# Kernel optimization log

Hardware: AMD Instinct MI355X
Metric: run time of the kernel (lower is better)

The kernel has to match this reference:

```python
import jax, jax.numpy as jnp
import numpy as np

T, B, D, H = 512, 64, 512, 512  # seq_len, batch, input_size, hidden_size


def setup_inputs() -> dict:
    key = jax.random.key(0)
    ks = jax.random.split(key, 7)
    s = 1.0 / np.sqrt(H)
    return {
        "input": jax.random.normal(ks[0], (T, B, D), dtype=jnp.float32),
        "h0": jax.random.normal(ks[1], (B, H), dtype=jnp.float32),
        "c0": jax.random.normal(ks[2], (B, H), dtype=jnp.float32),
        "W_ih": jax.random.normal(ks[3], (4 * H, D), dtype=jnp.float32) * s,
        "W_hh": jax.random.normal(ks[4], (4 * H, H), dtype=jnp.float32) * s,
        "b_ih": jax.random.normal(ks[5], (4 * H,), dtype=jnp.float32) * s,
        "b_hh": jax.random.normal(ks[6], (4 * H,), dtype=jnp.float32) * s,
        "batch_first": 0,
    }


def reference(input, h0, c0, W_ih, W_hh, b_ih, b_hh, batch_first):
    # Dense (non-packed) branch of RNNLayer.forward with an LSTM cell.
    x = jnp.swapaxes(input, 0, 1) if batch_first else input  # [T, B, D]
    # Input projection is independent of the recurrence: precompute for all t.
    x_proj = jnp.einsum('tbd,gd->tbg', x, W_ih) + b_ih  # [T, B, 4H]

    def step(carry, xt):
        h, c = carry
        gates = xt + h @ W_hh.T + b_hh  # [B, 4H]
        i, f, g, o = jnp.split(gates, 4, axis=-1)
        c_new = jax.nn.sigmoid(f) * c + jax.nn.sigmoid(i) * jnp.tanh(g)
        h_new = jax.nn.sigmoid(o) * jnp.tanh(c_new)
        return (h_new, c_new), h_new

    (hT, cT), ys = jax.lax.scan(step, (h0, c0), x_proj)  # ys: [T, B, H]
    outputs = jnp.swapaxes(ys, 0, 1) if batch_first else ys
    return outputs, hT, cT
```

## Files before the change

### kernel.cpp

```cpp
#include <hip/hip_runtime.h>

typedef __attribute__((ext_vector_type(8))) short bfrag;
typedef __attribute__((ext_vector_type(4))) float f32x4;
typedef __attribute__((ext_vector_type(4))) int i32x4;

#define NT 512
#define NB 64
#define KD 512
#define NG 2048
#define GB 4
#define GH 16

#define YS_SZ (NT * NB * KD)
#define HT_OFF YS_SZ
#define CT_OFF (YS_SZ + NB * KD)

__device__ __forceinline__ unsigned short f2bf(float f) {
  unsigned u = __float_as_uint(f);
  u += 0x7fffu + ((u >> 16) & 1u);
  return (unsigned short)(u >> 16);
}
__device__ __forceinline__ float bf2f(unsigned short h) {
  return __uint_as_float(((unsigned)h) << 16);
}
__device__ __forceinline__ float sigm(float v) { return 1.f / (1.f + __expf(-v)); }
__device__ __forceinline__ float tanh_f(float v) { return 1.f - 2.f / (__expf(2.f * v) + 1.f); }

__global__ __launch_bounds__(256) void cvt_bf16(const float* __restrict__ src,
                                                unsigned short* __restrict__ dst, int n8) {
  int i = blockIdx.x * 256 + threadIdx.x;
  if (i >= n8) return;
  const float4 a = *(const float4*)(src + (size_t)i * 8);
  const float4 b = *(const float4*)(src + (size_t)i * 8 + 4);
  i32x4 v;
  v.x = (int)(f2bf(a.x) | ((unsigned)f2bf(a.y) << 16));
  v.y = (int)(f2bf(a.z) | ((unsigned)f2bf(a.w) << 16));
  v.z = (int)(f2bf(b.x) | ((unsigned)f2bf(b.y) << 16));
  v.w = (int)(f2bf(b.z) | ((unsigned)f2bf(b.w) << 16));
  *(i32x4*)(dst + (size_t)i * 8) = v;
}

template <int XP32>
__global__ __launch_bounds__(256) void xproj_gemm(const unsigned short* __restrict__ Wb,
                                                  const unsigned short* __restrict__ Xb,
                                                  const float* __restrict__ bias,
                                                  void* __restrict__ XPv) {
  __shared__ unsigned short Wt[64 * 40];
  __shared__ unsigned short Xt[64 * 40];
  const int tid = threadIdx.x;
  const int lane = tid & 63, wid = tid >> 6;
  const int g = lane >> 4, cc = lane & 15;
  const int n0 = blockIdx.x * 64;
  const int t = blockIdx.y;
  const size_t m0 = (size_t)t * 64;
  const int srow = tid >> 2, schunk = (tid & 3) * 8;

  f32x4 acc[4] = {};
  for (int kb = 0; kb < KD; kb += 32) {
    __syncthreads();
    *(i32x4*)&Wt[srow * 40 + schunk] = *(const i32x4*)(Wb + (size_t)(n0 + srow) * KD + kb + schunk);
    *(i32x4*)&Xt[srow * 40 + schunk] = *(const i32x4*)(Xb + (m0 + srow) * KD + kb + schunk);
    __syncthreads();
    bfrag af = *(const bfrag*)&Wt[(wid * 16 + cc) * 40 + g * 8];
#pragma unroll
    for (int mt = 0; mt < 4; ++mt) {
      bfrag bf = *(const bfrag*)&Xt[(mt * 16 + cc) * 40 + g * 8];
      acc[mt] = __builtin_amdgcn_mfma_f32_16x16x32_bf16(af, bf, acc[mt], 0, 0, 0);
    }
  }
  const int nl = wid * 16 + g * 4;
  float bi[4];
#pragma unroll
  for (int r = 0; r < 4; ++r) bi[r] = bias[n0 + nl + r];
#pragma unroll
  for (int mt = 0; mt < 4; ++mt) {
#pragma unroll
    for (int r = 0; r < 4; ++r) {
      float v = acc[mt][r] + bi[r];
      size_t idx = ((size_t)t * NG + n0 + nl + r) * 64 + mt * 16 + cc;
      if (XP32) ((float*)XPv)[idx] = v;
      else ((unsigned short*)XPv)[idx] = f2bf(v);
    }
  }
}

template <int XP32>
__global__ __launch_bounds__(256, 1) void lstm_rec(const unsigned short* __restrict__ Whh,
                                                   const void* __restrict__ XPv,
                                                   const float* __restrict__ bhh,
                                                   const float* __restrict__ h0,
                                                   const float* __restrict__ c0,
                                                   unsigned short* __restrict__ hbuf,
                                                   unsigned int* __restrict__ bar,
                                                   float* __restrict__ out) {
  __shared__ unsigned short hl[16 * 512];
  __shared__ float hf[16 * 33];

  const int tid = threadIdx.x;
  const int lane = tid & 63, wid = tid >> 6;
  const int g = lane >> 4, cc = lane & 15;
  const int blk = blockIdx.x >> 4, slice = blockIdx.x & 15;
  const int b0 = blk * 16, d0 = slice * 32;
  unsigned int* flags = bar + blk * 64;
  unsigned long long* hb64 = (unsigned long long*)hbuf;

  if (tid < 128) {
    const int b = tid >> 3, dg = (tid & 7) * 4;
    const float* hsrc = h0 + (size_t)(b0 + b) * KD + d0 + dg;
    unsigned long long pk = (unsigned long long)f2bf(hsrc[0]) |
                            ((unsigned long long)f2bf(hsrc[1]) << 16) |
                            ((unsigned long long)f2bf(hsrc[2]) << 32) |
                            ((unsigned long long)f2bf(hsrc[3]) << 48);
    size_t ui = ((size_t)(b0 + b) * KD + d0 + dg) >> 2;
    __hip_atomic_store(hb64 + ui, pk, __ATOMIC_RELAXED, __HIP_MEMORY_SCOPE_AGENT);
  }
  asm volatile("s_waitcnt vmcnt(0)" ::: "memory");
  __syncthreads();
  if (tid == 0)
    __hip_atomic_store(flags + slice, 1u, __ATOMIC_RELAXED, __HIP_MEMORY_SCOPE_AGENT);

  bfrag w[2][16];
#pragma unroll
  for (int j = 0; j < 2; ++j) {
    const int tt = wid * 2 + j;
    const int r = tt * 16 + cc;
    const size_t n = (size_t)(r & 3) * KD + d0 + (r >> 2);
#pragma unroll
    for (int ks = 0; ks < 16; ++ks)
      w[j][ks] = *(const bfrag*)(Whh + n * KD + ks * 32 + g * 8);
  }
  float bh[2][4], creg[2];
#pragma unroll
  for (int j = 0; j < 2; ++j) {
    const int d = d0 + (wid * 2 + j) * 4 + g;
#pragma unroll
    for (int r = 0; r < 4; ++r) bh[j][r] = bhh[r * KD + d];
    creg[j] = c0[(b0 + cc) * KD + d];
  }

  for (int t = 0; t < NT; ++t) {
    float xp[2][4];
#pragma unroll
    for (int j = 0; j < 2; ++j) {
      const int d = d0 + (wid * 2 + j) * 4 + g;
#pragma unroll
      for (int r = 0; r < 4; ++r) {
        size_t idx = ((size_t)t * NG + r * KD + d) * 64 + b0 + cc;
        xp[j][r] = XP32 ? ((const float*)XPv)[idx] : bf2f(((const unsigned short*)XPv)[idx]);
      }
    }
    if (wid == 0) {
      const unsigned tgt = (unsigned)(t + 1);
      for (;;) {
        unsigned f = tgt;
        if (lane < 16)
          f = __hip_atomic_load(flags + lane, __ATOMIC_RELAXED, __HIP_MEMORY_SCOPE_AGENT);
        if (__all(f >= tgt)) break;
      }
    }
    __syncthreads();
    {
      const unsigned long long* hp =
          hb64 + (size_t)(t & 1) * (NB * KD / 4) + (size_t)b0 * (KD / 4);
      unsigned long long hv8[8];
#pragma unroll
      for (int j = 0; j < 8; ++j)
        hv8[j] = __hip_atomic_load(hp + j * 256 + tid, __ATOMIC_RELAXED, __HIP_MEMORY_SCOPE_AGENT);
#pragma unroll
      for (int j = 0; j < 8; ++j) {
        const int row = j * 2 + (tid >> 7);
        const int colb = (tid & 127) * 8;
        *(unsigned long long*)((char*)hl + row * 1024 + (colb ^ ((row & 7) << 4))) = hv8[j];
      }
    }
    __syncthreads();
    f32x4 acc0 = {0.f, 0.f, 0.f, 0.f}, acc1 = {0.f, 0.f, 0.f, 0.f};
#pragma unroll
    for (int ks = 0; ks < 16; ++ks) {
      const int off = ks * 64 + g * 16;
      bfrag hb = *(const bfrag*)((const char*)hl + cc * 1024 + (off ^ ((cc & 7) << 4)));
      acc0 = __builtin_amdgcn_mfma_f32_16x16x32_bf16(w[0][ks], hb, acc0, 0, 0, 0);
      acc1 = __builtin_amdgcn_mfma_f32_16x16x32_bf16(w[1][ks], hb, acc1, 0, 0, 0);
    }
#pragma unroll
    for (int j = 0; j < 2; ++j) {
      const f32x4 a = j ? acc1 : acc0;
      const int tt = wid * 2 + j;
      const int dl = tt * 4 + g;
      float gi = a[0] + xp[j][0] + bh[j][0];
      float gf = a[1] + xp[j][1] + bh[j][1];
      float gg = a[2] + xp[j][2] + bh[j][2];
      float go = a[3] + xp[j][3] + bh[j][3];
      float cn = sigm(gf) * creg[j] + sigm(gi) * tanh_f(gg);
      float hn = sigm(go) * tanh_f(cn);
      creg[j] = cn;
      hf[cc * 33 + dl] = hn;
      if (t == NT - 1) out[CT_OFF + (size_t)(b0 + cc) * KD + d0 + dl] = cn;
    }
    __syncthreads();
    float4 hv;
    if (tid < 128) {
      const int b = tid >> 3, dg = (tid & 7) * 4;
      hv.x = hf[b * 33 + dg];
      hv.y = hf[b * 33 + dg + 1];
      hv.z = hf[b * 33 + dg + 2];
      hv.w = hf[b * 33 + dg + 3];
      unsigned long long pk = (unsigned long long)f2bf(hv.x) |
                              ((unsigned long long)f2bf(hv.y) << 16) |
                              ((unsigned long long)f2bf(hv.z) << 32) |
                              ((unsigned long long)f2bf(hv.w) << 48);
      size_t ui = ((size_t)((t + 1) & 1) * NB * KD + (size_t)(b0 + b) * KD + d0 + dg) >> 2;
      __hip_atomic_store(hb64 + ui, pk, __ATOMIC_RELAXED, __HIP_MEMORY_SCOPE_AGENT);
    }
    asm volatile("s_waitcnt vmcnt(0)" ::: "memory");
    __syncthreads();
    if (tid == 0)
      __hip_atomic_store(flags + slice, (unsigned)(t + 2), __ATOMIC_RELAXED,
                         __HIP_MEMORY_SCOPE_AGENT);
    if (tid < 128) {
      const int b = tid >> 3, dg = (tid & 7) * 4;
      *(float4*)(out + (size_t)t * NB * KD + (size_t)(b0 + b) * KD + d0 + dg) = hv;
      if (t == NT - 1)
        *(float4*)(out + HT_OFF + (size_t)(b0 + b) * KD + d0 + dg) = hv;
    }
  }
}

extern "C" void kernel_launch(void* const* d_in, const int* in_sizes, int n_in,
                              void* d_out, int out_size, void* d_ws, size_t ws_size,
                              hipStream_t stream) {
  const float* x = (const float*)d_in[0];
  const float* h0 = (const float*)d_in[1];
  const float* c0 = (const float*)d_in[2];
  const float* Wih = (const float*)d_in[3];
  const float* Whh = (const float*)d_in[4];
  const float* bih = (const float*)d_in[5];
  const float* bhh = (const float*)d_in[6];
  float* out = (float*)d_out;
  char* ws = (char*)d_ws;

  unsigned int* bar = (unsigned int*)ws;
  unsigned short* hbuf = (unsigned short*)(ws + 4096);
  unsigned short* WhhB = (unsigned short*)(ws + 4096 + 131072);
  unsigned short* WihB = (unsigned short*)(ws + 4096 + 131072 + 2097152);
  unsigned short* XB = (unsigned short*)(ws + 4096 + 131072 + 2 * 2097152);
  const size_t xp_off = 4096 + 131072 + 2ull * 2097152 + 33554432;
  void* XP = (void*)(ws + xp_off);
  const bool xp32 = ws_size >= xp_off + (size_t)NT * NG * 64 * 4;

  hipMemsetAsync(ws, 0, 4096, stream);

  const int nx8 = NT * NB * KD / 8;
  const int nw8 = NG * KD / 8;
  cvt_bf16<<<dim3(nx8 / 256), 256, 0, stream>>>(x, XB, nx8);
  cvt_bf16<<<dim3(nw8 / 256), 256, 0, stream>>>(Wih, WihB, nw8);
  cvt_bf16<<<dim3(nw8 / 256), 256, 0, stream>>>(Whh, WhhB, nw8);

  if (xp32) {
    xproj_gemm<1><<<dim3(NG / 64, NT), 256, 0, stream>>>(WihB, XB, bih, XP);
    lstm_rec<1><<<dim3(GB * GH), 256, 0, stream>>>(WhhB, XP, bhh, h0, c0, hbuf, bar, out);
  } else {
    xproj_gemm<0><<<dim3(NG / 64, NT), 256, 0, stream>>>(WihB, XB, bih, XP);
    lstm_rec<0><<<dim3(GB * GH), 256, 0, stream>>>(WhhB, XP, bhh, h0, c0, hbuf, bar, out);
  }
}
```

Baseline: 1.638 ms.

## Add fast-path mailbox with sc0 loads and dual flags for inter-block h exchange

Reworks the per-step cross-block hidden-state exchange. It adds a fast mailbox written with plain stores and read with sc0 loads (likely hitting the shared XCD L2), plus a fallback device-scope mailbox and flags used after a bounded spin times out. The grid is doubled and half the blocks exit immediately, so the 16 slices of each batch group likely land on the same XCD under round-robin placement. The change also writes h directly from registers via a shuffle, splits the MFMA accumulation into two chains, and overlaps the flag updates with the stores. This relies on assumptions about block-to-XCD placement and cache coherence.

Result: slower. 2.164 ms (+32.1%).

```diff
diff --git a/kernel.cpp b/kernel.cpp
--- a/kernel.cpp
+++ b/kernel.cpp
@@ -14,6 +14,9 @@
 #define YS_SZ (NT * NB * KD)
 #define HT_OFF YS_SZ
 #define CT_OFF (YS_SZ + NB * KD)
+
+#define MB_BLK_ELEMS 8192
+#define MB_PAR_ELEMS (GB * MB_BLK_ELEMS)
 
 __device__ __forceinline__ unsigned short f2bf(float f) {
   unsigned u = __float_as_uint(f);
@@ -90,19 +93,24 @@
                                                    const float* __restrict__ bhh,
                                                    const float* __restrict__ h0,
                                                    const float* __restrict__ c0,
-                                                   unsigned short* __restrict__ hbuf,
-                                                   unsigned int* __restrict__ bar,
+                                                   unsigned short* __restrict__ mbf,
+                                                   unsigned short* __restrict__ mbs,
+                                                   unsigned int* __restrict__ ff,
+                                                   unsigned int* __restrict__ fs,
                                                    float* __restrict__ out) {
+  if ((blockIdx.x & 7) >= GB) return;
+
   __shared__ unsigned short hl[16 * 512];
   __shared__ float hf[16 * 33];
+  __shared__ unsigned mode_s;
 
   const int tid = threadIdx.x;
   const int lane = tid & 63, wid = tid >> 6;
   const int g = lane >> 4, cc = lane & 15;
-  const int blk = blockIdx.x >> 4, slice = blockIdx.x & 15;
+  const int blk = blockIdx.x & 7, slice = blockIdx.x >> 3;
   const int b0 = blk * 16, d0 = slice * 32;
-  unsigned int* flags = bar + blk * 64;
-  unsigned long long* hb64 = (unsigned long long*)hbuf;
+  unsigned int* flagf = ff + blk * 64;
+  unsigned int* flags = fs + blk * 64;
 
   if (tid < 128) {
     const int b = tid >> 3, dg = (tid & 7) * 4;
@@ -111,13 +119,16 @@
                             ((unsigned long long)f2bf(hsrc[1]) << 16) |
                             ((unsigned long long)f2bf(hsrc[2]) << 32) |
                             ((unsigned long long)f2bf(hsrc[3]) << 48);
-    size_t ui = ((size_t)(b0 + b) * KD + d0 + dg) >> 2;
-    __hip_atomic_store(hb64 + ui, pk, __ATOMIC_RELAXED, __HIP_MEMORY_SCOPE_AGENT);
-  }
-  asm volatile("s_waitcnt vmcnt(0)" ::: "memory");
+    const size_t ei = (size_t)blk * MB_BLK_ELEMS + b * KD + d0 + dg;
+    *(unsigned long long*)(mbf + ei) = pk;
+    __hip_atomic_store((unsigned long long*)(mbs + ei), pk, __ATOMIC_RELAXED,
+                       __HIP_MEMORY_SCOPE_AGENT);
+  }
   __syncthreads();
-  if (tid == 0)
-    __hip_atomic_store(flags + slice, 1u, __ATOMIC_RELAXED, __HIP_MEMORY_SCOPE_AGENT);
+  if (tid == 0) {
+    flagf[slice] = 1u;
+    __hip_atomic_store(&flags[slice], 1u, __ATOMIC_RELAXED, __HIP_MEMORY_SCOPE_AGENT);
+  }
 
   bfrag w[2][16];
 #pragma unroll
@@ -138,6 +149,8 @@
     creg[j] = c0[(b0 + cc) * KD + d];
   }
 
+  int slowcnt = 0;
+
   for (int t = 0; t < NT; ++t) {
     float xp[2][4];
 #pragma unroll
@@ -149,23 +162,69 @@
         xp[j][r] = XP32 ? ((const float*)XPv)[idx] : bf2f(((const unsigned short*)XPv)[idx]);
       }
     }
+    const unsigned tgt = (unsigned)(t + 1);
     if (wid == 0) {
-      const unsigned tgt = (unsigned)(t + 1);
-      for (;;) {
-        unsigned f = tgt;
-        if (lane < 16)
-          f = __hip_atomic_load(flags + lane, __ATOMIC_RELAXED, __HIP_MEMORY_SCOPE_AGENT);
-        if (__all(f >= tgt)) break;
-      }
+      bool done = false;
+      if (slowcnt < 3) {
+        for (int it = 0; it < 32 && !done; ++it) {
+          unsigned f = tgt;
+          if (lane < 16) {
+            const unsigned int* fp = flagf + lane;
+            asm volatile("global_load_dword %0, %1, off sc0\n\ts_waitcnt vmcnt(0)"
+                         : "=&v"(f) : "v"(fp) : "memory");
+          }
+          done = __all((f - tgt) <= 1u);
+        }
+      }
+      unsigned mode = 0;
+      if (!done) {
+        ++slowcnt;
+        mode = 1;
+        for (;;) {
+          unsigned f = tgt;
+          if (lane < 16)
+            f = __hip_atomic_load(flags + lane, __ATOMIC_RELAXED, __HIP_MEMORY_SCOPE_AGENT);
+          if (__all((f - tgt) <= 1u)) break;
+        }
+      } else {
+        slowcnt = 0;
+      }
+      if (tid == 0) mode_s = mode;
     }
     __syncthreads();
-    {
+    const unsigned mode = mode_s;
+    if (mode == 0) {
+      const char* pb = (const char*)(mbf + (size_t)(t & 1) * MB_PAR_ELEMS +
+                                     (size_t)blk * MB_BLK_ELEMS);
+      i32x4 va, vb, vc, vd;
+      asm volatile(
+          "global_load_dwordx4 %0, %4, off sc0\n\t"
+          "global_load_dwordx4 %1, %5, off sc0\n\t"
+          "global_load_dwordx4 %2, %6, off sc0\n\t"
+          "global_load_dwordx4 %3, %7, off sc0\n\t"
+          "s_waitcnt vmcnt(0)"
+          : "=&v"(va), "=&v"(vb), "=&v"(vc), "=&v"(vd)
+          : "v"(pb + tid * 16), "v"(pb + tid * 16 + 4096),
+            "v"(pb + tid * 16 + 8192), "v"(pb + tid * 16 + 12288)
+          : "memory");
+      __builtin_amdgcn_sched_barrier(0);
+      const int colb = (tid * 16) & 1023;
+      const int r0 = tid >> 6;
+#pragma unroll
+      for (int j = 0; j < 4; ++j) {
+        const int row = r0 + j * 4;
+        *(i32x4*)((char*)hl + row * 1024 + (colb ^ ((row & 7) << 4))) =
+            (j == 0) ? va : (j == 1) ? vb : (j == 2) ? vc : vd;
+      }
+    } else {
       const unsigned long long* hp =
-          hb64 + (size_t)(t & 1) * (NB * KD / 4) + (size_t)b0 * (KD / 4);
+          (const unsigned long long*)(mbs + (size_t)(t & 1) * MB_PAR_ELEMS +
+                                      (size_t)blk * MB_BLK_ELEMS);
       unsigned long long hv8[8];
 #pragma unroll
       for (int j = 0; j < 8; ++j)
-        hv8[j] = __hip_atomic_load(hp + j * 256 + tid, __ATOMIC_RELAXED, __HIP_MEMORY_SCOPE_AGENT);
+        hv8[j] = __hip_atomic_load(hp + j * 256 + tid, __ATOMIC_RELAXED,
+                                   __HIP_MEMORY_SCOPE_AGENT);
 #pragma unroll
       for (int j = 0; j < 8; ++j) {
         const int row = j * 2 + (tid >> 7);
@@ -174,51 +233,72 @@
       }
     }
     __syncthreads();
-    f32x4 acc0 = {0.f, 0.f, 0.f, 0.f}, acc1 = {0.f, 0.f, 0.f, 0.f};
-#pragma unroll
-    for (int ks = 0; ks < 16; ++ks) {
+    f32x4 p00 = {0.f, 0.f, 0.f, 0.f}, p01 = {0.f, 0.f, 0.f, 0.f};
+    f32x4 p10 = {0.f, 0.f, 0.f, 0.f}, p11 = {0.f, 0.f, 0.f, 0.f};
+#pragma unroll
+    for (int ks = 0; ks < 8; ++ks) {
       const int off = ks * 64 + g * 16;
       bfrag hb = *(const bfrag*)((const char*)hl + cc * 1024 + (off ^ ((cc & 7) << 4)));
-      acc0 = __builtin_amdgcn_mfma_f32_16x16x32_bf16(w[0][ks], hb, acc0, 0, 0, 0);
-      acc1 = __builtin_amdgcn_mfma_f32_16x16x32_bf16(w[1][ks], hb, acc1, 0, 0, 0);
-    }
+      p00 = __builtin_amdgcn_mfma_f32_16x16x32_bf16(w[0][ks], hb, p00, 0, 0, 0);
+      p10 = __builtin_amdgcn_mfma_f32_16x16x32_bf16(w[1][ks], hb, p10, 0, 0, 0);
+    }
+#pragma unroll
+    for (int ks = 8; ks < 16; ++ks) {
+      const int off = ks * 64 + g * 16;
+      bfrag hb = *(const bfrag*)((const char*)hl + cc * 1024 + (off ^ ((cc & 7) << 4)));
+      p01 = __builtin_amdgcn_mfma_f32_16x16x32_bf16(w[0][ks], hb, p01, 0, 0, 0);
+      p11 = __builtin_amdgcn_mfma_f32_16x16x32_bf16(w[1][ks], hb, p11, 0, 0, 0);
+    }
+    const f32x4 acc0 = p00 + p01, acc1 = p10 + p11;
+    float hnv[2];
 #pragma unroll
     for (int j = 0; j < 2; ++j) {
       const f32x4 a = j ? acc1 : acc0;
-      const int tt = wid * 2 + j;
-      const int dl = tt * 4 + g;
       float gi = a[0] + xp[j][0] + bh[j][0];
       float gf = a[1] + xp[j][1] + bh[j][1];
       float gg = a[2] + xp[j][2] + bh[j][2];
       float go = a[3] + xp[j][3] + bh[j][3];
       float cn = sigm(gf) * creg[j] + sigm(gi) * tanh_f(gg);
-      float hn = sigm(go) * tanh_f(cn);
       creg[j] = cn;
-      hf[cc * 33 + dl] = hn;
-      if (t == NT - 1) out[CT_OFF + (size_t)(b0 + cc) * KD + d0 + dl] = cn;
-    }
-    __syncthreads();
-    float4 hv;
+      hnv[j] = sigm(go) * tanh_f(cn);
+      if (t == NT - 1) out[CT_OFF + (size_t)(b0 + cc) * KD + d0 + (wid * 8 + j * 4 + g)] = cn;
+    }
+    {
+      unsigned short* fb = mbf + (size_t)((t + 1) & 1) * MB_PAR_ELEMS + (size_t)blk * MB_BLK_ELEMS;
+      unsigned short* sb = mbs + (size_t)((t + 1) & 1) * MB_PAR_ELEMS + (size_t)blk * MB_BLK_ELEMS;
+      const float o0 = __shfl_xor(hnv[0], 16);
+      const float o1 = __shfl_xor(hnv[1], 16);
+      if (!(g & 1)) {
+        const unsigned w0 = (unsigned)f2bf(hnv[0]) | ((unsigned)f2bf(o0) << 16);
+        const unsigned w1 = (unsigned)f2bf(hnv[1]) | ((unsigned)f2bf(o1) << 16);
+        const int e0 = cc * KD + d0 + wid * 8 + g;
+        const int e1 = e0 + 4;
+        *(unsigned*)(fb + e0) = w0;
+        *(unsigned*)(fb + e1) = w1;
+        asm volatile("" ::: "memory");
+        __hip_atomic_store((unsigned*)(sb + e0), w0, __ATOMIC_RELAXED, __HIP_MEMORY_SCOPE_AGENT);
+        __hip_atomic_store((unsigned*)(sb + e1), w1, __ATOMIC_RELAXED, __HIP_MEMORY_SCOPE_AGENT);
+      }
+    }
+    hf[cc * 33 + wid * 8 + g] = hnv[0];
+    hf[cc * 33 + wid * 8 + 4 + g] = hnv[1];
+    asm volatile("s_waitcnt vmcnt(2) lgkmcnt(0)" ::: "memory");
+    __builtin_amdgcn_sched_barrier(0);
+    __builtin_amdgcn_s_barrier();
+    if (tid == 0) flagf[slice] = (unsigned)(t + 2);
+    asm volatile("s_waitcnt vmcnt(0)" ::: "memory");
+    __builtin_amdgcn_sched_barrier(0);
+    __builtin_amdgcn_s_barrier();
+    if (tid == 0)
+      __hip_atomic_store(&flags[slice], (unsigned)(t + 2), __ATOMIC_RELAXED,
+                         __HIP_MEMORY_SCOPE_AGENT);
     if (tid < 128) {
       const int b = tid >> 3, dg = (tid & 7) * 4;
+      float4 hv;
       hv.x = hf[b * 33 + dg];
       hv.y = hf[b * 33 + dg + 1];
       hv.z = hf[b * 33 + dg + 2];
       hv.w = hf[b * 33 + dg + 3];
-      unsigned long long pk = (unsigned long long)f2bf(hv.x) |
-                              ((unsigned long long)f2bf(hv.y) << 16) |
-                              ((unsigned long long)f2bf(hv.z) << 32) |
-                              ((unsigned long long)f2bf(hv.w) << 48);
-      size_t ui = ((size_t)((t + 1) & 1) * NB * KD + (size_t)(b0 + b) * KD + d0 + dg) >> 2;
-      __hip_atomic_store(hb64 + ui, pk, __ATOMIC_RELAXED, __HIP_MEMORY_SCOPE_AGENT);
-    }
-    asm volatile("s_waitcnt vmcnt(0)" ::: "memory");
-    __syncthreads();
-    if (tid == 0)
-      __hip_atomic_store(flags + slice, (unsigned)(t + 2), __ATOMIC_RELAXED,
-                         __HIP_MEMORY_SCOPE_AGENT);
-    if (tid < 128) {
-      const int b = tid >> 3, dg = (tid & 7) * 4;
       *(float4*)(out + (size_t)t * NB * KD + (size_t)(b0 + b) * KD + d0 + dg) = hv;
       if (t == NT - 1)
         *(float4*)(out + HT_OFF + (size_t)(b0 + b) * KD + d0 + dg) = hv;
@@ -239,16 +319,18 @@
   float* out = (float*)d_out;
   char* ws = (char*)d_ws;
 
-  unsigned int* bar = (unsigned int*)ws;
-  unsigned short* hbuf = (unsigned short*)(ws + 4096);
-  unsigned short* WhhB = (unsigned short*)(ws + 4096 + 131072);
-  unsigned short* WihB = (unsigned short*)(ws + 4096 + 131072 + 2097152);
-  unsigned short* XB = (unsigned short*)(ws + 4096 + 131072 + 2 * 2097152);
-  const size_t xp_off = 4096 + 131072 + 2ull * 2097152 + 33554432;
+  unsigned int* ff = (unsigned int*)ws;
+  unsigned int* fs = (unsigned int*)(ws + 4096);
+  unsigned short* mbf = (unsigned short*)(ws + 8192);
+  unsigned short* mbs = (unsigned short*)(ws + 8192 + 131072);
+  unsigned short* WhhB = (unsigned short*)(ws + 270336);
+  unsigned short* WihB = (unsigned short*)(ws + 270336 + 2097152);
+  unsigned short* XB = (unsigned short*)(ws + 270336 + 2 * 2097152);
+  const size_t xp_off = 270336 + 2ull * 2097152 + 33554432;
   void* XP = (void*)(ws + xp_off);
   const bool xp32 = ws_size >= xp_off + (size_t)NT * NG * 64 * 4;
 
-  hipMemsetAsync(ws, 0, 4096, stream);
+  hipMemsetAsync(ws, 0, 8192, stream);
 
   const int nx8 = NT * NB * KD / 8;
   const int nw8 = NG * KD / 8;
@@ -258,9 +340,9 @@
 
   if (xp32) {
     xproj_gemm<1><<<dim3(NG / 64, NT), 256, 0, stream>>>(WihB, XB, bih, XP);
-    lstm_rec<1><<<dim3(GB * GH), 256, 0, stream>>>(WhhB, XP, bhh, h0, c0, hbuf, bar, out);
+    lstm_rec<1><<<dim3(GB * GH * 2), 256, 0, stream>>>(WhhB, XP, bhh, h0, c0, mbf, mbs, ff, fs, out);
   } else {
     xproj_gemm<0><<<dim3(NG / 64, NT), 256, 0, stream>>>(WihB, XB, bih, XP);
-    lstm_rec<0><<<dim3(GB * GH), 256, 0, stream>>>(WhhB, XP, bhh, h0, c0, hbuf, bar, out);
-  }
-}
+    lstm_rec<0><<<dim3(GB * GH * 2), 256, 0, stream>>>(WhhB, XP, bhh, h0, c0, mbf, mbs, ff, fs, out);
+  }
+}
```
